# Kernel tuning notes

Measured on AMD Instinct MI355X. Metric: run time of the kernel, lower is better.

Reference implementation:

```python
import jax, jax.numpy as jnp
import numpy as np

IN_CH = 128
OUT_CH = 128
N_NODES = 20000
N_EDGES = 320000
EPS = 1e-5


def setup_inputs() -> dict:
    key = jax.random.key(0)
    ks = jax.random.split(key, 8)
    node_embeddings = jax.random.normal(ks[0], (N_NODES, IN_CH), dtype=jnp.float32)
    edge_index = jax.random.randint(ks[1], (2, N_EDGES), 0, N_NODES, dtype=jnp.int64)
    s = 1.0 / np.sqrt(IN_CH)
    W1 = jax.random.uniform(ks[2], (IN_CH, IN_CH), jnp.float32, -s, s)
    b1 = jax.random.uniform(ks[3], (IN_CH,), jnp.float32, -s, s)
    W2 = jax.random.uniform(ks[4], (IN_CH, IN_CH), jnp.float32, -s, s)
    b2 = jax.random.uniform(ks[5], (IN_CH,), jnp.float32, -s, s)
    sm = 1.0 / np.sqrt(2 * IN_CH)
    Wm = jax.random.uniform(ks[6], (2 * IN_CH, 2 * OUT_CH), jnp.float32, -sm, sm)
    bm = jax.random.uniform(ks[7], (2 * OUT_CH,), jnp.float32, -sm, sm)
    gamma = jnp.ones((OUT_CH,), jnp.float32)
    beta = jnp.zeros((OUT_CH,), jnp.float32)
    return {"node_embeddings": node_embeddings, "edge_index": edge_index,
            "W1": W1, "b1": b1, "W2": W2, "b2": b2,
            "Wm": Wm, "bm": bm, "gamma": gamma, "beta": beta}


def reference(node_embeddings, edge_index, W1, b1, W2, b2, Wm, bm, gamma, beta):
    # gather endpoint embeddings: [E, d]
    src = node_embeddings[edge_index[0]]
    dst = node_embeddings[edge_index[1]]
    src_emb = src @ W1 + b1                       # Linear v1
    dst_emb = dst @ W2 + b2                       # Linear v2
    edge_attr = jnp.concatenate([src_emb, dst_emb], axis=-1)  # [E, 2d]
    h = edge_attr @ Wm + bm                       # [E, 2*out]
    x, gate = jnp.split(h, 2, axis=-1)            # GeGLU (exact gelu, torch default)
    y = x * jax.nn.gelu(gate, approximate=False)  # [E, out]
    mu = jnp.mean(y, axis=-1, keepdims=True)
    var = jnp.var(y, axis=-1, keepdims=True)
    y_norm = (y - mu) * jax.lax.rsqrt(var + EPS)
    return y_norm * gamma + beta
```

## Files before the change

kernel.cpp:

```cpp
#include <hip/hip_runtime.h>
#include <hip/hip_fp16.h>
#include <math.h>


#define CH 128
#define NB 32
#define BCAP 10496
#define SCHUNK 2048

typedef _Float16 half8 __attribute__((ext_vector_type(8)));
typedef float floatx4 __attribute__((ext_vector_type(4)));

__device__ __forceinline__ int permcol(int j2) {
  int c = j2 & 127;
  int isg = j2 >> 7;
  return ((c >> 1) << 2) | (isg << 1) | (c & 1);
}

__global__ __launch_bounds__(256) void prep_scatter_kernel(
    const float* __restrict__ W1, const float* __restrict__ b1,
    const float* __restrict__ W2, const float* __restrict__ b2,
    const float* __restrict__ Wm, const float* __restrict__ bm,
    __half* __restrict__ CcatT, float* __restrict__ dvec,
    const int* __restrict__ eidx, int E, int npb,
    unsigned int* __restrict__ cursor,
    int2* __restrict__ sorted) {
  const int bid = blockIdx.x;
  const int tid = threadIdx.x;
  if (bid < 256) {
    int idx = bid * 256 + tid;
    int i = idx >> 9;
    int j = idx & 511;
    int jc = j & 255;
    const float* wrow = (j < 256) ? (W1 + i * CH) : (W2 + i * CH);
    const float* wm   = (j < 256) ? (Wm + jc) : (Wm + CH * 256 + jc);
    float acc = 0.f;
#pragma unroll 8
    for (int k = 0; k < CH; ++k) acc = fmaf(wrow[k], wm[k * 256], acc);
    int scol = (j & 256) | permcol(j & 255);
    CcatT[scol * CH + i] = __float2half(acc);
    return;
  }
  if (bid == 256) {
    if (tid < 256) {
      float acc = bm[tid];
#pragma unroll 8
      for (int k = 0; k < CH; ++k) {
        acc = fmaf(b1[k], Wm[k * 256 + tid], acc);
        acc = fmaf(b2[k], Wm[(CH + k) * 256 + tid], acc);
      }
      dvec[permcol(tid)] = acc;
    }
    return;
  }
  __shared__ unsigned int lcnt[NB], lbase[NB], loff[NB];
  const int c0 = (bid - 257) * SCHUNK;
  if (tid < NB) { lcnt[tid] = 0; loff[tid] = 0; }
  __syncthreads();
  int svals[SCHUNK / 256], dvals[SCHUNK / 256];
  signed char kvals[SCHUNK / 256];
#pragma unroll
  for (int r = 0; r < SCHUNK / 256; ++r) {
    int e = c0 + r * 256 + tid;
    int k = -1, s = 0, d = 0;
    if (e < E) {
      s = eidx[e]; d = eidx[E + e];
      k = s / npb;
      atomicAdd(&lcnt[k], 1u);
    }
    svals[r] = s; dvals[r] = d; kvals[r] = (signed char)k;
  }
  __syncthreads();
  if (tid < NB) {
    unsigned int c = lcnt[tid];
    lbase[tid] = c ? ((unsigned int)tid * BCAP + atomicAdd(&cursor[tid], c))
                   : 0u;
  }
  __syncthreads();
#pragma unroll
  for (int r = 0; r < SCHUNK / 256; ++r) {
    int e = c0 + r * 256 + tid;
    if (e < E) {
      int k = (int)kvals[r];
      unsigned int pos = lbase[k] + atomicAdd(&loff[k], 1u);
      sorted[pos] = make_int2(e, svals[r] | (dvals[r] << 15));
    }
  }
}

__global__ __launch_bounds__(256) void node_gemm(
    const float* __restrict__ A,
    const __half* __restrict__ BT,
    __half* __restrict__ C,
    int M) {
  __shared__ __align__(16) _Float16 As[64 * 136];
  __shared__ __align__(16) _Float16 Bs[64 * 136];
  const int tid = threadIdx.x;
  const int row0 = blockIdx.x * 64;
  const int col0 = blockIdx.y * 64;

#pragma unroll
  for (int rnd = 0; rnd < 4; ++rnd) {
    int idx = (tid + rnd * 256) * 8;
    int r = idx >> 7, c = idx & 127;
    int rg = row0 + r; if (rg >= M) rg = M - 1;
    float4 v0 = *(const float4*)(A + (size_t)rg * CH + c);
    float4 v1 = *(const float4*)(A + (size_t)rg * CH + c + 4);
    __half2 h0 = __floats2half2_rn(v0.x, v0.y);
    __half2 h1 = __floats2half2_rn(v0.z, v0.w);
    __half2 h2 = __floats2half2_rn(v1.x, v1.y);
    __half2 h3 = __floats2half2_rn(v1.z, v1.w);
    uint4 u;
    u.x = *(const unsigned int*)&h0; u.y = *(const unsigned int*)&h1;
    u.z = *(const unsigned int*)&h2; u.w = *(const unsigned int*)&h3;
    *(uint4*)(As + r * 136 + c) = u;
    uint4 w4 = *(const uint4*)(BT + (size_t)(col0 + r) * CH + c);
    *(uint4*)(Bs + r * 136 + c) = w4;
  }
  __syncthreads();

  const int w = tid >> 6, l = tid & 63;
  const int mr = w * 16 + (l & 15);
  const int kq = (l >> 4) * 8;

  half8 a[4];
#pragma unroll
  for (int kc = 0; kc < 4; ++kc)
    a[kc] = *(const half8*)(As + mr * 136 + kc * 32 + kq);

  floatx4 acc[4] = {{0,0,0,0},{0,0,0,0},{0,0,0,0},{0,0,0,0}};
#pragma unroll
  for (int kc = 0; kc < 4; ++kc) {
#pragma unroll
    for (int nb = 0; nb < 4; ++nb) {
      half8 b = *(const half8*)(Bs + (nb * 16 + (l & 15)) * 136 + kc * 32 + kq);
      acc[nb] = __builtin_amdgcn_mfma_f32_16x16x32_f16(a[kc], b, acc[nb], 0, 0, 0);
    }
  }

  const int colb = col0 + (l & 15);
  const int rowb = row0 + w * 16 + (l >> 4) * 4;
#pragma unroll
  for (int nb = 0; nb < 4; ++nb) {
#pragma unroll
    for (int rg = 0; rg < 4; ++rg) {
      int row = rowb + rg;
      if (row < M)
        C[(size_t)row * 512 + colb + nb * 16] = __float2half(acc[nb][rg]);
    }
  }
}

__device__ __forceinline__ float gelu_t(float g) {
  float g2 = g * g;
  float t = g * fmaf(g2, 0.10294515f, 2.3021858f);
  float u = exp2f(t);
  return g * u * __builtin_amdgcn_rcpf(1.0f + u);
}

__device__ __forceinline__ void process_edge(
    uint4 pu, uint4 qu, float4 dv0, float4 dv1, float4 gm, float4 bt,
    float* __restrict__ outp, int hl) {
  __half2 sx01 = __hadd2(*(const __half2*)&pu.x, *(const __half2*)&qu.x);
  __half2 sg01 = __hadd2(*(const __half2*)&pu.y, *(const __half2*)&qu.y);
  __half2 sx23 = __hadd2(*(const __half2*)&pu.z, *(const __half2*)&qu.z);
  __half2 sg23 = __hadd2(*(const __half2*)&pu.w, *(const __half2*)&qu.w);
  float2 x01 = __half22float2(sx01);
  float2 g01 = __half22float2(sg01);
  float2 x23 = __half22float2(sx23);
  float2 g23 = __half22float2(sg23);

  float x0 = x01.x + dv0.x, x1 = x01.y + dv0.y;
  float g0 = g01.x + dv0.z, g1 = g01.y + dv0.w;
  float x2 = x23.x + dv1.x, x3 = x23.y + dv1.y;
  float g2 = g23.x + dv1.z, g3 = g23.y + dv1.w;

  float y0 = x0 * gelu_t(g0);
  float y1 = x1 * gelu_t(g1);
  float y2 = x2 * gelu_t(g2);
  float y3 = x3 * gelu_t(g3);

  float s1 = (y0 + y1) + (y2 + y3);
  float s2 = fmaf(y0, y0, fmaf(y1, y1, fmaf(y2, y2, y3 * y3)));
#pragma unroll
  for (int off = 16; off; off >>= 1) {
    s1 += __shfl_xor(s1, off, 64);
    s2 += __shfl_xor(s2, off, 64);
  }
  float mu  = s1 * (1.0f / 128.0f);
  float var = s2 * (1.0f / 128.0f) - mu * mu;
  float rstd = rsqrtf(var + 1e-5f);

  float4 o;
  o.x = fmaf((y0 - mu) * rstd, gm.x, bt.x);
  o.y = fmaf((y1 - mu) * rstd, gm.y, bt.y);
  o.z = fmaf((y2 - mu) * rstd, gm.z, bt.z);
  o.w = fmaf((y3 - mu) * rstd, gm.w, bt.w);
  *(float4*)(outp + hl * 4) = o;
}

__global__ __launch_bounds__(256) void edge_kernel(
    const __half* __restrict__ PQ,
    const float* __restrict__ dvec,
    const float* __restrict__ gamma,
    const float* __restrict__ beta,
    const unsigned int* __restrict__ cursor,
    const int2* __restrict__ sorted,
    float* __restrict__ out) {
  const int per = gridDim.x >> 3;
  const int nb2 = (blockIdx.x & 7) * per + (blockIdx.x >> 3);
  const int wave = threadIdx.x >> 6;
  const int lane = threadIdx.x & 63;
  const int hl = lane & 31;
  const int side = lane >> 5;
  const int i0 = nb2 * 16 + wave * 4 + side;

  const int slotA = i0, slotB = i0 + 2;
  const int bA = slotA / BCAP, bB = slotB / BCAP;
  const bool vA = (unsigned int)(slotA - bA * BCAP) < cursor[bA];
  const bool vB = (unsigned int)(slotB - bB * BCAP) < cursor[bB];
  if (!vA && !vB) return;

  float4 dv0 = *(const float4*)(dvec + hl * 8);
  float4 dv1 = *(const float4*)(dvec + hl * 8 + 4);
  float4 gm  = *(const float4*)(gamma + hl * 4);
  float4 bt  = *(const float4*)(beta + hl * 4);

  int eA = 0, sA = 0, dA = 0, eB = 0, sB = 0, dB = 0;
  if (vA) { int2 pk = sorted[slotA]; eA = pk.x; sA = pk.y & 0x7fff; dA = pk.y >> 15; }
  if (vB) { int2 pk = sorted[slotB]; eB = pk.x; sB = pk.y & 0x7fff; dB = pk.y >> 15; }

  const char* pqb = (const char*)PQ;
  uint4 puA = *(const uint4*)(pqb + (size_t)sA * 1024 + hl * 16);
  uint4 quA = *(const uint4*)(pqb + (size_t)dA * 1024 + 512 + hl * 16);
  uint4 puB = *(const uint4*)(pqb + (size_t)sB * 1024 + hl * 16);
  uint4 quB = *(const uint4*)(pqb + (size_t)dB * 1024 + 512 + hl * 16);

  if (vA)
    process_edge(puA, quA, dv0, dv1, gm, bt, out + (size_t)eA * CH, hl);
  if (vB)
    process_edge(puB, quB, dv0, dv1, gm, bt, out + (size_t)eB * CH, hl);
}

extern "C" void kernel_launch(void* const* d_in, const int* in_sizes, int n_in,
                              void* d_out, int out_size, void* d_ws, size_t ws_size,
                              hipStream_t stream) {
  const float* emb   = (const float*)d_in[0];
  const int*   eidx  = (const int*)d_in[1];
  const float* W1    = (const float*)d_in[2];
  const float* b1    = (const float*)d_in[3];
  const float* W2    = (const float*)d_in[4];
  const float* b2    = (const float*)d_in[5];
  const float* Wm    = (const float*)d_in[6];
  const float* bm    = (const float*)d_in[7];
  const float* gamma = (const float*)d_in[8];
  const float* beta  = (const float*)d_in[9];

  const int M = in_sizes[0] / CH;
  const int E = in_sizes[1] / 2;
  const int npb = (M + NB - 1) / NB;

  float*        dvec   = (float*)d_ws;
  unsigned int* cursor = (unsigned int*)(dvec + 256);
  __half*       CcatT  = (__half*)(cursor + 64);
  int2*         sorted = (int2*)(CcatT + 512 * CH);
  __half*       PQ     = (__half*)(sorted + NB * BCAP);

  hipMemsetAsync(cursor, 0, NB * sizeof(unsigned int), stream);

  const int nchunks = (E + SCHUNK - 1) / SCHUNK;
  prep_scatter_kernel<<<257 + nchunks, 256, 0, stream>>>(
      W1, b1, W2, b2, Wm, bm, CcatT, dvec, eidx, E, npb, cursor, sorted);

  dim3 g2((M + 63) / 64, 512 / 64);
  node_gemm<<<g2, 256, 0, stream>>>(emb, CcatT, PQ, M);

  const int nslots = NB * BCAP;
  edge_kernel<<<nslots / 16, 256, 0, stream>>>(PQ, dvec, gamma, beta, cursor,
                                               sorted, (float*)d_out);
}
```

Before: 85.82 us.

## Co-schedule edge scatter with node GEMM and use 16-lane DPP edge processing

Moves the edge bucket-scatter blocks out of the weight-prep kernel and into the node GEMM launch, so the scatter runs alongside the GEMM instead of alongside the small prep work. The edge kernel now gives each edge 16 lanes that each handle 8 channels, and does the LayerNorm reduction with DPP row operations instead of shuffles. The aim is to balance the grids and cut per-edge reduction and instruction overhead. In exchange, the GEMM blocks now carry extra shared memory for the scatter counters, and each lane holds more registers.

```diff
diff --git a/kernel.cpp b/kernel.cpp
--- a/kernel.cpp
+++ b/kernel.cpp
@@ -17,14 +17,11 @@
   return ((c >> 1) << 2) | (isg << 1) | (c & 1);
 }
 
-__global__ __launch_bounds__(256) void prep_scatter_kernel(
+__global__ __launch_bounds__(256) void prep_kernel(
     const float* __restrict__ W1, const float* __restrict__ b1,
     const float* __restrict__ W2, const float* __restrict__ b2,
     const float* __restrict__ Wm, const float* __restrict__ bm,
-    __half* __restrict__ CcatT, float* __restrict__ dvec,
-    const int* __restrict__ eidx, int E, int npb,
-    unsigned int* __restrict__ cursor,
-    int2* __restrict__ sorted) {
+    __half* __restrict__ CcatT, float* __restrict__ dvec) {
   const int bid = blockIdx.x;
   const int tid = threadIdx.x;
   if (bid < 256) {
@@ -39,65 +36,70 @@
     for (int k = 0; k < CH; ++k) acc = fmaf(wrow[k], wm[k * 256], acc);
     int scol = (j & 256) | permcol(j & 255);
     CcatT[scol * CH + i] = __float2half(acc);
-    return;
-  }
-  if (bid == 256) {
-    if (tid < 256) {
-      float acc = bm[tid];
+  } else if (tid < 256) {
+    float acc = bm[tid];
 #pragma unroll 8
-      for (int k = 0; k < CH; ++k) {
-        acc = fmaf(b1[k], Wm[k * 256 + tid], acc);
-        acc = fmaf(b2[k], Wm[(CH + k) * 256 + tid], acc);
-      }
-      dvec[permcol(tid)] = acc;
-    }
-    return;
-  }
-  __shared__ unsigned int lcnt[NB], lbase[NB], loff[NB];
-  const int c0 = (bid - 257) * SCHUNK;
-  if (tid < NB) { lcnt[tid] = 0; loff[tid] = 0; }
-  __syncthreads();
-  int svals[SCHUNK / 256], dvals[SCHUNK / 256];
-  signed char kvals[SCHUNK / 256];
-#pragma unroll
-  for (int r = 0; r < SCHUNK / 256; ++r) {
-    int e = c0 + r * 256 + tid;
-    int k = -1, s = 0, d = 0;
-    if (e < E) {
-      s = eidx[e]; d = eidx[E + e];
-      k = s / npb;
-      atomicAdd(&lcnt[k], 1u);
-    }
-    svals[r] = s; dvals[r] = d; kvals[r] = (signed char)k;
-  }
-  __syncthreads();
-  if (tid < NB) {
-    unsigned int c = lcnt[tid];
-    lbase[tid] = c ? ((unsigned int)tid * BCAP + atomicAdd(&cursor[tid], c))
-                   : 0u;
-  }
-  __syncthreads();
-#pragma unroll
-  for (int r = 0; r < SCHUNK / 256; ++r) {
-    int e = c0 + r * 256 + tid;
-    if (e < E) {
-      int k = (int)kvals[r];
-      unsigned int pos = lbase[k] + atomicAdd(&loff[k], 1u);
-      sorted[pos] = make_int2(e, svals[r] | (dvals[r] << 15));
-    }
-  }
-}
-
-__global__ __launch_bounds__(256) void node_gemm(
+    for (int k = 0; k < CH; ++k) {
+      acc = fmaf(b1[k], Wm[k * 256 + tid], acc);
+      acc = fmaf(b2[k], Wm[(CH + k) * 256 + tid], acc);
+    }
+    dvec[permcol(tid)] = acc;
+  }
+}
+
+__global__ __launch_bounds__(256) void gemm_scatter_kernel(
     const float* __restrict__ A,
     const __half* __restrict__ BT,
     __half* __restrict__ C,
-    int M) {
+    int M, int nscatter,
+    const int* __restrict__ eidx, int E, int npb,
+    unsigned int* __restrict__ cursor,
+    int2* __restrict__ sorted) {
   __shared__ __align__(16) _Float16 As[64 * 136];
   __shared__ __align__(16) _Float16 Bs[64 * 136];
+  __shared__ unsigned int lcnt[NB], lbase[NB], loff[NB];
+  const int bid = blockIdx.x;
   const int tid = threadIdx.x;
-  const int row0 = blockIdx.x * 64;
-  const int col0 = blockIdx.y * 64;
+
+  if (bid < nscatter) {
+    const int c0 = bid * SCHUNK;
+    if (tid < NB) { lcnt[tid] = 0; loff[tid] = 0; }
+    __syncthreads();
+    int svals[SCHUNK / 256], dvals[SCHUNK / 256];
+    signed char kvals[SCHUNK / 256];
+#pragma unroll
+    for (int r = 0; r < SCHUNK / 256; ++r) {
+      int e = c0 + r * 256 + tid;
+      int k = -1, s = 0, d = 0;
+      if (e < E) {
+        s = eidx[e]; d = eidx[E + e];
+        k = s / npb;
+        atomicAdd(&lcnt[k], 1u);
+      }
+      svals[r] = s; dvals[r] = d; kvals[r] = (signed char)k;
+    }
+    __syncthreads();
+    if (tid < NB) {
+      unsigned int c = lcnt[tid];
+      lbase[tid] = c ? ((unsigned int)tid * BCAP + atomicAdd(&cursor[tid], c))
+                     : 0u;
+    }
+    __syncthreads();
+#pragma unroll
+    for (int r = 0; r < SCHUNK / 256; ++r) {
+      int e = c0 + r * 256 + tid;
+      if (e < E) {
+        int k = (int)kvals[r];
+        unsigned int pos = lbase[k] + atomicAdd(&loff[k], 1u);
+        sorted[pos] = make_int2(e, svals[r] | (dvals[r] << 15));
+      }
+    }
+    return;
+  }
+
+  const int g = bid - nscatter;
+  const int row0 = (g >> 3) * 64;
+  const int col0 = (g & 7) * 64;
 
 #pragma unroll
   for (int rnd = 0; rnd < 4; ++rnd) {
@@ -158,45 +160,18 @@
   return g * u * __builtin_amdgcn_rcpf(1.0f + u);
 }
 
-__device__ __forceinline__ void process_edge(
-    uint4 pu, uint4 qu, float4 dv0, float4 dv1, float4 gm, float4 bt,
-    float* __restrict__ outp, int hl) {
-  __half2 sx01 = __hadd2(*(const __half2*)&pu.x, *(const __half2*)&qu.x);
-  __half2 sg01 = __hadd2(*(const __half2*)&pu.y, *(const __half2*)&qu.y);
-  __half2 sx23 = __hadd2(*(const __half2*)&pu.z, *(const __half2*)&qu.z);
-  __half2 sg23 = __hadd2(*(const __half2*)&pu.w, *(const __half2*)&qu.w);
-  float2 x01 = __half22float2(sx01);
-  float2 g01 = __half22float2(sg01);
-  float2 x23 = __half22float2(sx23);
-  float2 g23 = __half22float2(sg23);
-
-  float x0 = x01.x + dv0.x, x1 = x01.y + dv0.y;
-  float g0 = g01.x + dv0.z, g1 = g01.y + dv0.w;
-  float x2 = x23.x + dv1.x, x3 = x23.y + dv1.y;
-  float g2 = g23.x + dv1.z, g3 = g23.y + dv1.w;
-
-  float y0 = x0 * gelu_t(g0);
-  float y1 = x1 * gelu_t(g1);
-  float y2 = x2 * gelu_t(g2);
-  float y3 = x3 * gelu_t(g3);
-
-  float s1 = (y0 + y1) + (y2 + y3);
-  float s2 = fmaf(y0, y0, fmaf(y1, y1, fmaf(y2, y2, y3 * y3)));
-#pragma unroll
-  for (int off = 16; off; off >>= 1) {
-    s1 += __shfl_xor(s1, off, 64);
-    s2 += __shfl_xor(s2, off, 64);
-  }
-  float mu  = s1 * (1.0f / 128.0f);
-  float var = s2 * (1.0f / 128.0f) - mu * mu;
-  float rstd = rsqrtf(var + 1e-5f);
-
-  float4 o;
-  o.x = fmaf((y0 - mu) * rstd, gm.x, bt.x);
-  o.y = fmaf((y1 - mu) * rstd, gm.y, bt.y);
-  o.z = fmaf((y2 - mu) * rstd, gm.z, bt.z);
-  o.w = fmaf((y3 - mu) * rstd, gm.w, bt.w);
-  *(float4*)(outp + hl * 4) = o;
+template <int CTRL>
+__device__ __forceinline__ float dpp_radd(float x) {
+  int t = __builtin_amdgcn_update_dpp(0, __float_as_int(x), CTRL, 0xf, 0xf,
+                                      true);
+  return x + __int_as_float(t);
+}
+__device__ __forceinline__ float row16_sum(float x) {
+  x = dpp_radd<0x128>(x);
+  x = dpp_radd<0x124>(x);
+  x = dpp_radd<0x122>(x);
+  x = dpp_radd<0x121>(x);
+  return x;
 }
 
 __global__ __launch_bounds__(256) void edge_kernel(
@@ -211,35 +186,79 @@
   const int nb2 = (blockIdx.x & 7) * per + (blockIdx.x >> 3);
   const int wave = threadIdx.x >> 6;
   const int lane = threadIdx.x & 63;
-  const int hl = lane & 31;
-  const int side = lane >> 5;
-  const int i0 = nb2 * 16 + wave * 4 + side;
-
-  const int slotA = i0, slotB = i0 + 2;
-  const int bA = slotA / BCAP, bB = slotB / BCAP;
-  const bool vA = (unsigned int)(slotA - bA * BCAP) < cursor[bA];
-  const bool vB = (unsigned int)(slotB - bB * BCAP) < cursor[bB];
-  if (!vA && !vB) return;
-
-  float4 dv0 = *(const float4*)(dvec + hl * 8);
-  float4 dv1 = *(const float4*)(dvec + hl * 8 + 4);
-  float4 gm  = *(const float4*)(gamma + hl * 4);
-  float4 bt  = *(const float4*)(beta + hl * 4);
-
-  int eA = 0, sA = 0, dA = 0, eB = 0, sB = 0, dB = 0;
-  if (vA) { int2 pk = sorted[slotA]; eA = pk.x; sA = pk.y & 0x7fff; dA = pk.y >> 15; }
-  if (vB) { int2 pk = sorted[slotB]; eB = pk.x; sB = pk.y & 0x7fff; dB = pk.y >> 15; }
+  const int grp = lane >> 4;
+  const int hl = lane & 15;
+  const int slot = nb2 * 16 + wave * 4 + grp;
+  const int b = slot / BCAP;
+  const bool v = (unsigned int)(slot - b * BCAP) < cursor[b];
+  if (__ballot(v) == 0) return;
+
+  int2 pk = v ? sorted[slot] : make_int2(0, 0);
+  const int e = pk.x;
+  const int s = pk.y & 0x7fff;
+  const int d = pk.y >> 15;
 
   const char* pqb = (const char*)PQ;
-  uint4 puA = *(const uint4*)(pqb + (size_t)sA * 1024 + hl * 16);
-  uint4 quA = *(const uint4*)(pqb + (size_t)dA * 1024 + 512 + hl * 16);
-  uint4 puB = *(const uint4*)(pqb + (size_t)sB * 1024 + hl * 16);
-  uint4 quB = *(const uint4*)(pqb + (size_t)dB * 1024 + 512 + hl * 16);
-
-  if (vA)
-    process_edge(puA, quA, dv0, dv1, gm, bt, out + (size_t)eA * CH, hl);
-  if (vB)
-    process_edge(puB, quB, dv0, dv1, gm, bt, out + (size_t)eB * CH, hl);
+  uint4 pu0 = *(const uint4*)(pqb + (size_t)s * 1024 + hl * 32);
+  uint4 pu1 = *(const uint4*)(pqb + (size_t)s * 1024 + hl * 32 + 16);
+  uint4 qu0 = *(const uint4*)(pqb + (size_t)d * 1024 + 512 + hl * 32);
+  uint4 qu1 = *(const uint4*)(pqb + (size_t)d * 1024 + 512 + hl * 32 + 16);
+
+  float4 dv0 = *(const float4*)(dvec + hl * 16);
+  float4 dv1 = *(const float4*)(dvec + hl * 16 + 4);
+  float4 dv2 = *(const float4*)(dvec + hl * 16 + 8);
+  float4 dv3 = *(const float4*)(dvec + hl * 16 + 12);
+  float4 gm0 = *(const float4*)(gamma + hl * 8);
+  float4 gm1 = *(const float4*)(gamma + hl * 8 + 4);
+  float4 bt0 = *(const float4*)(beta + hl * 8);
+  float4 bt1 = *(const float4*)(beta + hl * 8 + 4);
+
+  __half2 sx01 = __hadd2(*(const __half2*)&pu0.x, *(const __half2*)&qu0.x);
+  __half2 sg01 = __hadd2(*(const __half2*)&pu0.y, *(const __half2*)&qu0.y);
+  __half2 sx23 = __hadd2(*(const __half2*)&pu0.z, *(const __half2*)&qu0.z);
+  __half2 sg23 = __hadd2(*(const __half2*)&pu0.w, *(const __half2*)&qu0.w);
+  __half2 sx45 = __hadd2(*(const __half2*)&pu1.x, *(const __half2*)&qu1.x);
+  __half2 sg45 = __hadd2(*(const __half2*)&pu1.y, *(const __half2*)&qu1.y);
+  __half2 sx67 = __hadd2(*(const __half2*)&pu1.z, *(const __half2*)&qu1.z);
+  __half2 sg67 = __hadd2(*(const __half2*)&pu1.w, *(const __half2*)&qu1.w);
+  float2 x01 = __half22float2(sx01), g01 = __half22float2(sg01);
+  float2 x23 = __half22float2(sx23), g23 = __half22float2(sg23);
+  float2 x45 = __half22float2(sx45), g45 = __half22float2(sg45);
+  float2 x67 = __half22float2(sx67), g67 = __half22float2(sg67);
+
+  float y0 = (x01.x + dv0.x) * gelu_t(g01.x + dv0.z);
+  float y1 = (x01.y + dv0.y) * gelu_t(g01.y + dv0.w);
+  float y2 = (x23.x + dv1.x) * gelu_t(g23.x + dv1.z);
+  float y3 = (x23.y + dv1.y) * gelu_t(g23.y + dv1.w);
+  float y4 = (x45.x + dv2.x) * gelu_t(g45.x + dv2.z);
+  float y5 = (x45.y + dv2.y) * gelu_t(g45.y + dv2.w);
+  float y6 = (x67.x + dv3.x) * gelu_t(g67.x + dv3.z);
+  float y7 = (x67.y + dv3.y) * gelu_t(g67.y + dv3.w);
+
+  float s1 = ((y0 + y1) + (y2 + y3)) + ((y4 + y5) + (y6 + y7));
+  float s2 = fmaf(y0, y0, fmaf(y1, y1, fmaf(y2, y2, y3 * y3)));
+  s2 = fmaf(y4, y4, fmaf(y5, y5, fmaf(y6, y6, fmaf(y7, y7, s2))));
+  s1 = row16_sum(s1);
+  s2 = row16_sum(s2);
+
+  float mu  = s1 * (1.0f / 128.0f);
+  float var = s2 * (1.0f / 128.0f) - mu * mu;
+  float rstd = rsqrtf(var + 1e-5f);
+
+  float4 o0, o1;
+  o0.x = fmaf((y0 - mu) * rstd, gm0.x, bt0.x);
+  o0.y = fmaf((y1 - mu) * rstd, gm0.y, bt0.y);
+  o0.z = fmaf((y2 - mu) * rstd, gm0.z, bt0.z);
+  o0.w = fmaf((y3 - mu) * rstd, gm0.w, bt0.w);
+  o1.x = fmaf((y4 - mu) * rstd, gm1.x, bt1.x);
+  o1.y = fmaf((y5 - mu) * rstd, gm1.y, bt1.y);
+  o1.z = fmaf((y6 - mu) * rstd, gm1.z, bt1.z);
+  o1.w = fmaf((y7 - mu) * rstd, gm1.w, bt1.w);
+  if (v) {
+    float* outp = out + (size_t)e * CH + hl * 8;
+    *(float4*)outp = o0;
+    *(float4*)(outp + 4) = o1;
+  }
 }
 
 extern "C" void kernel_launch(void* const* d_in, const int* in_sizes, int n_in,
@@ -268,12 +287,12 @@
 
   hipMemsetAsync(cursor, 0, NB * sizeof(unsigned int), stream);
 
-  const int nchunks = (E + SCHUNK - 1) / SCHUNK;
-  prep_scatter_kernel<<<257 + nchunks, 256, 0, stream>>>(
-      W1, b1, W2, b2, Wm, bm, CcatT, dvec, eidx, E, npb, cursor, sorted);
-
-  dim3 g2((M + 63) / 64, 512 / 64);
-  node_gemm<<<g2, 256, 0, stream>>>(emb, CcatT, PQ, M);
+  prep_kernel<<<257, 256, 0, stream>>>(W1, b1, W2, b2, Wm, bm, CcatT, dvec);
+
+  const int nscatter = (E + SCHUNK - 1) / SCHUNK;
+  const int ngemm = ((M + 63) / 64) * 8;
+  gemm_scatter_kernel<<<nscatter + ngemm, 256, 0, stream>>>(
+      emb, CcatT, PQ, M, nscatter, eidx, E, npb, cursor, sorted);
 
   const int nslots = NB * BCAP;
   edge_kernel<<<nslots / 16, 256, 0, stream>>>(PQ, dvec, gamma, beta, cursor,
```

Result: slower. 90.41 us (+5.3%).
